# Kernel optimization log

Measured on AMD Instinct MI355X. Metric: run time of the kernel, lower is better.

## Reference

```python
import jax, jax.numpy as jnp
import numpy as np

B, N, HID = 1, 2048, 1024
H, WK, WV = 16, 64, 64
DH = HID // H  # 64


def setup_inputs() -> dict:
    key = jax.random.key(0)
    ks = jax.random.split(key, 10)
    s = 0.02
    return {
        "hidden_states": jax.random.normal(ks[0], (B, N, HID), jnp.float32),
        "attention_mask": jnp.ones((B, N), jnp.float32),
        "Wq": jax.random.normal(ks[1], (HID, HID), jnp.float32) * s,
        "bq": jnp.zeros((HID,), jnp.float32),
        "Wk": jax.random.normal(ks[2], (HID, HID), jnp.float32) * s,
        "bk": jnp.zeros((HID,), jnp.float32),
        "Wv": jax.random.normal(ks[3], (HID, HID), jnp.float32) * s,
        "bv": jnp.zeros((HID,), jnp.float32),
        # Conv1D(2*WK+1, DH, bias=False): weight [nx=DH, nf=2*WK+1]
        "W_rel_k": jax.random.normal(ks[4], (DH, 2 * WK + 1), jnp.float32) * s,
        # relative_pos_val: [2*WV+1, DH]
        "W_rel_v": jax.random.normal(ks[5], (2 * WV + 1, DH), jnp.float32) * s,
    }


def _attention(hidden_states, attention_mask, Wq, bq, Wk, bk, Wv, bv, W_rel_k, W_rel_v):
    b, n, _ = hidden_states.shape

    def heads(x):  # [B,N,HID] -> [B,H,N,DH]
        return x.reshape(b, n, H, DH).transpose(0, 2, 1, 3)

    q = heads(hidden_states @ Wq + bq)
    k = heads(hidden_states @ Wk + bk)
    v = heads(hidden_states @ Wv + bv)

    scores = jnp.einsum("bhid,bhjd->bhij", q, k)  # [B,H,N,N]

    # --- relative-position key bias: bias[i, j] = q_i . w_{j-i+WK} for |j-i|<=WK ---
    a_k = jnp.einsum("bhid,dw->bhiw", q, W_rel_k)  # [B,H,N,2*WK+1]
    rows = jnp.arange(n)
    slot = rows[None, :] - rows[:, None] + WK       # [N,N] relative slot j-i+WK
    valid_k = (slot >= 0) & (slot <= 2 * WK)
    bias = a_k[:, :, rows[:, None], jnp.clip(slot, 0, 2 * WK)]  # [B,H,N,N]
    scores = scores + jnp.where(valid_k, bias, 0.0)

    scores = scores / np.float32(np.sqrt(DH))  # temperature == 1.0

    # extended attention mask: (1 - mask) * dtype_min added to scores
    ext = (1.0 - attention_mask)[:, None, None, :] * jnp.finfo(scores.dtype).min
    scores = scores + ext

    probs = jax.nn.softmax(scores, axis=-1)  # [B,H,N,N]

    ctx = jnp.einsum("bhij,bhjd->bhid", probs, v)  # [B,H,N,DH]

    # --- relative-position value: band[i, r] = probs[i, i-WV+r]; ctx += band @ W_rel_v ---
    offs = jnp.arange(2 * WV + 1)
    kpos = rows[:, None] - WV + offs[None, :]       # [N, 2*WV+1] absolute key position
    valid_v = (kpos >= 0) & (kpos < n)
    band = probs[:, :, rows[:, None], jnp.clip(kpos, 0, n - 1)]  # [B,H,N,2*WV+1]
    band = jnp.where(valid_v, band, 0.0)
    ctx = ctx + jnp.einsum("bhiw,wd->bhid", band, W_rel_v)

    # merge heads -> [B,N,HID]
    return ctx.transpose(0, 2, 1, 3).reshape(b, n, HID)


def reference(hidden_states, attention_mask, Wq, bq, Wk, bk, Wv, bv, W_rel_k, W_rel_v):
    return _attention(hidden_states, attention_mask, Wq, bq, Wk, bk, Wv, bv, W_rel_k, W_rel_v)
```

## Files before the change

### kernel.cpp

```cpp
#include <hip/hip_runtime.h>
#include <hip/hip_bf16.h>

#define NSEQ 2048
#define HIDDIM 1024
#define NH 16
#define DHEAD 64
#define NW 129
#define AKS 132

typedef float          f32x4 __attribute__((ext_vector_type(4)));
typedef _Float16       f16x4 __attribute__((ext_vector_type(4)));
typedef _Float16       f16x8 __attribute__((ext_vector_type(8)));
typedef unsigned short u16x8 __attribute__((ext_vector_type(8)));
typedef unsigned short u16;

__device__ __forceinline__ float b2f(u16 u){ return __uint_as_float(((unsigned)u) << 16); }
__device__ __forceinline__ float ld_any(const void* p, long idx, int flag){
  return flag ? b2f(((const u16*)p)[idx]) : ((const float*)p)[idx];
}
__device__ __forceinline__ int dtype_flag(const void* mask){
  return (((const unsigned*)mask)[0] == 0x3F800000u) ? 0 : 1;
}

#define GLOAD_LDS16(gp, lp) \
  __builtin_amdgcn_global_load_lds((const __attribute__((address_space(1))) unsigned int*)(gp), \
                                   (__attribute__((address_space(3))) unsigned int*)(lp), 16, 0, 0)

static const size_t OFF_Q    = 0;
static const size_t OFF_K    = (size_t)4  << 20;
static const size_t OFF_VT   = (size_t)8  << 20;
static const size_t OFF_WT   = (size_t)12 << 20;
static const size_t OFF_AK   = (size_t)18 << 20;
static const size_t OFF_M    = OFF_AK + (size_t)NH * NSEQ * AKS * 4;
static const size_t OFF_L    = OFF_M + (size_t)2 * NH * NSEQ * 4;
static const size_t OFF_CTXP = OFF_L + (size_t)2 * NH * NSEQ * 4;
static const size_t OFF_HSF  = OFF_CTXP + (size_t)2 * NSEQ * HIDDIM * 4;
static const size_t OFF_BIAS = OFF_HSF + (size_t)NSEQ * HIDDIM * 2;
static const size_t OFF_EXT  = OFF_BIAS + 3 * 1024 * 4;
static const size_t OFF_WRKT = OFF_EXT + (size_t)NSEQ * 4;
static const size_t OFF_WRVT = OFF_WRKT + (size_t)144 * 72 * 2;

__global__ void prep_kernel(const void* __restrict__ hs, const void* __restrict__ mask,
                            const void* __restrict__ bq, const void* __restrict__ bk,
                            const void* __restrict__ bv, const void* __restrict__ wrk,
                            const void* __restrict__ wrv,
                            const void* __restrict__ Wq, const void* __restrict__ Wk,
                            const void* __restrict__ Wv,
                            _Float16* __restrict__ hsf, float* __restrict__ biasf,
                            float* __restrict__ extf, _Float16* __restrict__ wrkT16,
                            _Float16* __restrict__ wrvT16, _Float16* __restrict__ Wt){
  __shared__ __attribute__((aligned(16))) _Float16 tile[64][65];
  const int flag = dtype_flag(mask);
  const int b = blockIdx.x;
  const int t = threadIdx.x;
  if (b < 1024){
    const long base = (long)(b * 256 + t) * 8;
    f16x8 o;
    if (flag){
      u16x8 v = *(const u16x8*)((const u16*)hs + base);
#pragma unroll
      for (int e = 0; e < 8; e++) o[e] = (_Float16)b2f(v[e]);
    } else {
      f32x4 a = *(const f32x4*)((const float*)hs + base);
      f32x4 c = *(const f32x4*)((const float*)hs + base + 4);
#pragma unroll
      for (int e = 0; e < 4; e++){ o[e] = (_Float16)a[e]; o[4 + e] = (_Float16)c[e]; }
    }
    *(f16x8*)(hsf + base) = o;
    return;
  }
  if (b < 1121){
    const int idx = (b - 1024) * 256 + t;
    if (idx < 1024)            biasf[idx] = ld_any(bq, idx, flag);
    else if (idx < 2048)       biasf[idx] = ld_any(bk, idx - 1024, flag);
    else if (idx < 3072)       biasf[idx] = ld_any(bv, idx - 2048, flag);
    else if (idx < 5120)       extf[idx - 3072] = (1.f - ld_any(mask, idx - 3072, flag)) * -1.0e30f;
    else if (idx < 5120 + 144 * 72){
      int i2 = idx - 5120;
      int w = i2 / 72, d = i2 - w * 72;
      wrkT16[i2] = (w < NW && d < 64) ? (_Float16)ld_any(wrk, (long)d * NW + w, flag) : (_Float16)0.f;
    } else if (idx < 5120 + 144 * 72 + 64 * 144){
      int i3 = idx - (5120 + 144 * 72);
      int d = i3 / 144, w = i3 - d * 144;
      wrvT16[i3] = (w < NW) ? (_Float16)ld_any(wrv, (long)w * 64 + d, flag) : (_Float16)0.f;
    }
    return;
  }
  const int b2 = b - 1121;
  const int z = b2 >> 8, rem = b2 & 255;
  const void* src = (z == 0) ? Wq : ((z == 1) ? Wk : Wv);
  _Float16* dst = Wt + (size_t)z * 1024 * 1024;
  const int o0 = (rem & 15) * 64, k0 = (rem >> 4) * 64;
#pragma unroll
  for (int c = 0; c < 2; c++){
    int idx = t + 256 * c;
    int r = idx >> 3, c8 = (idx & 7) * 8;
    long off = (long)(k0 + r) * 1024 + o0 + c8;
    if (flag){
      u16x8 v = *(const u16x8*)((const u16*)src + off);
#pragma unroll
      for (int e = 0; e < 8; e++) tile[r][c8 + e] = (_Float16)b2f(v[e]);
    } else {
      f32x4 a = *(const f32x4*)((const float*)src + off);
      f32x4 bb = *(const f32x4*)((const float*)src + off + 4);
#pragma unroll
      for (int e = 0; e < 4; e++){ tile[r][c8 + e] = (_Float16)a[e]; tile[r][c8 + 4 + e] = (_Float16)bb[e]; }
    }
  }
  __syncthreads();
#pragma unroll
  for (int c = 0; c < 2; c++){
    int idx = t + 256 * c;
    int orow = idx >> 3, k8 = (idx & 7) * 8;
    f16x8 v;
#pragma unroll
    for (int e = 0; e < 8; e++) v[e] = tile[k8 + e][orow];
    *(f16x8*)(dst + (size_t)(o0 + orow) * 1024 + k0 + k8) = v;
  }
}

__launch_bounds__(512, 4)
__global__ void qkv_kernel(const _Float16* __restrict__ hsf, const _Float16* __restrict__ Wt,
                           const float* __restrict__ biasf, const _Float16* __restrict__ wrkT16,
                           _Float16* __restrict__ Qf, _Float16* __restrict__ Kf,
                           _Float16* __restrict__ Vtf, float* __restrict__ akp){
  __shared__ __attribute__((aligned(16))) _Float16 As[2 * 64 * 64];
  __shared__ __attribute__((aligned(16))) _Float16 Bs[2 * 128 * 64];
  const int z = blockIdx.z;
  const _Float16* Wz = Wt + (size_t)z * 1024 * 1024;
  const int o0 = blockIdx.x * 128, m0 = blockIdx.y * 64;
  const int t = threadIdx.x, lane = t & 63, wave = t >> 6;
  const int wm = wave >> 2, wn = wave & 3;
  const int q = lane >> 4, ln = lane & 15;

  auto stage = [&](int nb, int k0){
    {
      const int row = t >> 3, slot = t & 7;
      const int c8 = slot ^ (row & 7);
      GLOAD_LDS16(hsf + (size_t)(m0 + row) * 1024 + k0 + (c8 << 3),
                  (_Float16*)As + nb * 4096 + (wave << 9));
    }
#pragma unroll
    for (int p = 0; p < 2; p++){
      const int g = p * 512 + t;
      const int row = g >> 3, slot = g & 7;
      const int c8 = slot ^ (row & 7);
      GLOAD_LDS16(Wz + (size_t)(o0 + row) * 1024 + k0 + (c8 << 3),
                  (_Float16*)Bs + nb * 8192 + ((p * 8 + wave) << 9));
    }
  };

  f32x4 acc[2][2];
#pragma unroll
  for (int a = 0; a < 2; a++)
#pragma unroll
    for (int b = 0; b < 2; b++) acc[a][b] = (f32x4){0.f, 0.f, 0.f, 0.f};

  stage(0, 0);
  __syncthreads();
  int cur = 0;
  for (int k0 = 0; k0 < 1024; k0 += 64){
    if (k0 + 64 < 1024) stage(cur ^ 1, k0 + 64);
    const _Float16* Ac = (const _Float16*)As + cur * 4096;
    const _Float16* Bc = (const _Float16*)Bs + cur * 8192;
    __builtin_amdgcn_s_setprio(1);
#pragma unroll
    for (int ks = 0; ks < 2; ks++){
      f16x8 af[2], bf[2];
#pragma unroll
      for (int mt = 0; mt < 2; mt++){
        int row = wm * 32 + mt * 16 + ln;
        af[mt] = *(const f16x8*)&Ac[(row << 6) + (((ks * 4 + q) ^ (row & 7)) << 3)];
      }
#pragma unroll
      for (int nt = 0; nt < 2; nt++){
        int row = wn * 32 + nt * 16 + ln;
        bf[nt] = *(const f16x8*)&Bc[(row << 6) + (((ks * 4 + q) ^ (row & 7)) << 3)];
      }
#pragma unroll
      for (int mt = 0; mt < 2; mt++)
#pragma unroll
        for (int nt = 0; nt < 2; nt++)
          acc[mt][nt] = __builtin_amdgcn_mfma_f32_16x16x32_f16(af[mt], bf[nt], acc[mt][nt], 0, 0, 0);
    }
    __builtin_amdgcn_s_setprio(0);
    __syncthreads();
    cur ^= 1;
  }
  const float sc = (z == 0) ? 0.125f : 1.0f;
  _Float16* Qs = (_Float16*)As;
  _Float16* Wl = (_Float16*)Bs;
#pragma unroll
  for (int nt = 0; nt < 2; nt++){
    int ol = wn * 32 + nt * 16 + ln;
    int o = o0 + ol;
    float bval = biasf[z * 1024 + o];
    int hh = o >> 6, dd = o & 63;
#pragma unroll
    for (int mt = 0; mt < 2; mt++){
      int ml = wm * 32 + mt * 16 + q * 4;
      int nb = m0 + ml;
      if (z == 2){
        f16x4 pk;
#pragma unroll
        for (int r = 0; r < 4; r++) pk[r] = (_Float16)(acc[mt][nt][r] + bval);
        *(f16x4*)(Vtf + (size_t)(hh * 64 + dd) * 2048 + nb) = pk;
      } else {
        _Float16* dstp = (z == 0) ? Qf : Kf;
#pragma unroll
        for (int r = 0; r < 4; r++){
          _Float16 v16 = (_Float16)((acc[mt][nt][r] + bval) * sc);
          dstp[(size_t)(hh * 2048 + nb + r) * 64 + dd] = v16;
          if (z == 0) Qs[(ol >> 6) * 4096 + (ml + r) * 64 + dd] = v16;
        }
      }
    }
  }
  if (z == 0){
    {
      const f16x8* srcv = (const f16x8*)wrkT16;
      f16x8* dstv = (f16x8*)Wl;
#pragma unroll
      for (int c = 0; c < 3; c++){
        int v = c * 512 + t;
        if (v < 144 * 72 / 8) dstv[v] = srcv[v];
      }
    }
    __syncthreads();
    const int hl = wave >> 2, mb = wave & 3;
    f16x8 afr[2];
#pragma unroll
    for (int ks = 0; ks < 2; ks++)
      afr[ks] = *(const f16x8*)&Qs[hl * 4096 + (mb * 16 + ln) * 64 + ks * 32 + q * 8];
    f32x4 aacc[9];
#pragma unroll
    for (int b = 0; b < 9; b++) aacc[b] = (f32x4){0.f, 0.f, 0.f, 0.f};
#pragma unroll
    for (int nt = 0; nt < 9; nt++){
      f16x8 bfr0 = *(const f16x8*)&Wl[(nt * 16 + ln) * 72 + q * 8];
      f16x8 bfr1 = *(const f16x8*)&Wl[(nt * 16 + ln) * 72 + 32 + q * 8];
      aacc[nt] = __builtin_amdgcn_mfma_f32_16x16x32_f16(afr[0], bfr0, aacc[nt], 0, 0, 0);
      aacc[nt] = __builtin_amdgcn_mfma_f32_16x16x32_f16(afr[1], bfr1, aacc[nt], 0, 0, 0);
    }
    const int hg = blockIdx.x * 2 + hl;
#pragma unroll
    for (int nt = 0; nt < 9; nt++){
      int w = nt * 16 + ln;
      if (w > 128) continue;
      int ib = m0 + mb * 16 + q * 4;
#pragma unroll
      for (int r = 0; r < 4; r++)
        akp[(size_t)(hg * 2048 + ib + r) * AKS + w] = aacc[nt][r];
    }
  }
}

__launch_bounds__(256, 4)
__global__ void flash_kernel(const float* __restrict__ extf,
                             const _Float16* __restrict__ Qf, const _Float16* __restrict__ Kf,
                             const _Float16* __restrict__ Vtf, float* akm,
                             _Float16* __restrict__ ctxpart, float* __restrict__ mws,
                             float* __restrict__ lws){
  __shared__ __attribute__((aligned(16))) _Float16 Ks[2 * 64 * 64];
  __shared__ __attribute__((aligned(16))) _Float16 Vts[2 * 64 * 64];
  __shared__ __attribute__((aligned(16))) float Exts[1024];
  __shared__ int eflags[4];
  const int h = blockIdx.x, qt = blockIdx.y, jh = blockIdx.z;
  const int t = threadIdx.x, lane = t & 63, wave = t >> 6;
  const int q = lane >> 4, ln = lane & 15;
  const int ibase = qt * 64 + wave * 16;
  const int i = ibase + ln;
  const int jb = jh * 1024;
  const int phase = (h + 3 * qt + 8 * jh) & 15;

  auto stageK = [&](int nb, int jn){
#pragma unroll
    for (int p = 0; p < 2; p++){
      const int g = p * 256 + t;
      const int row = g >> 3, slot = g & 7;
      const int col8 = slot ^ (row & 7);
      GLOAD_LDS16(Kf + (((size_t)(h * 2048 + jn + row)) << 6) + (col8 << 3),
                  (_Float16*)Ks + nb * 4096 + ((p * 4 + wave) << 9));
    }
  };
  auto stageV = [&](int nb, int jn){
#pragma unroll
    for (int p = 0; p < 2; p++){
      const int g = p * 256 + t;
      const int row = g >> 3, slot = g & 7;
      const int col8 = slot ^ (row & 7);
      GLOAD_LDS16(Vtf + (((size_t)(h * 64 + row)) << 11) + jn + (col8 << 3),
                  (_Float16*)Vts + nb * 4096 + ((p * 4 + wave) << 9));
    }
  };

  const int ds7 = ln & 7;
  const _Float16* kb0 = (const _Float16*)Ks + (ln << 6) + ((q ^ ds7) << 3);
  const _Float16* kb1 = (const _Float16*)Ks + (ln << 6) + (((q + 4) ^ ds7) << 3);
  const _Float16* vb0 = (const _Float16*)Vts + (ln << 6) + (((0 | (q >> 1)) ^ ds7) << 3) + ((q & 1) << 2);
  const _Float16* vb1 = (const _Float16*)Vts + (ln << 6) + (((2 | (q >> 1)) ^ ds7) << 3) + ((q & 1) << 2);
  const _Float16* vb2 = (const _Float16*)Vts + (ln << 6) + (((4 | (q >> 1)) ^ ds7) << 3) + ((q & 1) << 2);
  const _Float16* vb3 = (const _Float16*)Vts + (ln << 6) + (((6 | (q >> 1)) ^ ds7) << 3) + ((q & 1) << 2);

  f16x8 qfrag[2];
  {
    const _Float16* qrow = Qf + (size_t)(h * 2048 + i) * 64;
    qfrag[0] = *(const f16x8*)(qrow + q * 8);
    qfrag[1] = *(const f16x8*)(qrow + 32 + q * 8);
  }
  f32x4 accc[4];
#pragma unroll
  for (int dt = 0; dt < 4; dt++) accc[dt] = (f32x4){0.f, 0.f, 0.f, 0.f};
  float m_i = -1.0e30f, l_i = 0.f;
  float* akrow = akm + (size_t)(h * 2048 + i) * AKS;
  f32x4 s[4];

  auto qk = [&](int PK){
    __builtin_amdgcn_s_setprio(1);
#pragma unroll
    for (int mt = 0; mt < 4; mt++){
      f16x8 kf0 = *(const f16x8*)(kb0 + PK * 4096 + mt * 1024);
      f16x8 kf1 = *(const f16x8*)(kb1 + PK * 4096 + mt * 1024);
      f32x4 zz = (f32x4){0.f, 0.f, 0.f, 0.f};
      zz = __builtin_amdgcn_mfma_f32_16x16x32_f16(kf0, qfrag[0], zz, 0, 0, 0);
      zz = __builtin_amdgcn_mfma_f32_16x16x32_f16(kf1, qfrag[1], zz, 0, 0, 0);
      s[mt] = zz;
    }
    __builtin_amdgcn_s_setprio(0);
  };

  auto jof = [&](int x){ return jb + ((x + phase) & 15) * 64; };

  bool nz = false;
#pragma unroll
  for (int c = 0; c < 4; c++){
    float e = extf[jb + c * 256 + t];
    Exts[c * 256 + t] = e;
    nz |= (e != 0.f);
  }
  {
    unsigned long long bz = __ballot(nz);
    if (lane == 0) eflags[wave] = (bz != 0ull) ? 1 : 0;
  }
  stageK(0, jof(0));
  __syncthreads();
  const bool extNZ = (eflags[0] | eflags[1] | eflags[2] | eflags[3]) != 0;
  stageV(0, jof(0));
  stageK(1, jof(1));
  qk(0);
  __syncthreads();

  auto body = [&](int t_, int PV_, int PK1, bool last){
    const int j0 = jof(t_);
    if (!last){
      stageV(PK1, jof(t_ + 1));
      if (t_ < 14) stageK(PV_, jof(t_ + 2));
    }
    const bool band = (j0 <= ibase + 79) && (j0 + 63 >= ibase - 64);
    const int je = (t_ + phase) & 15;
    if (band){
#pragma unroll
      for (int mt = 0; mt < 4; mt++){
        f32x4 ev = *(const f32x4*)&Exts[je * 64 + mt * 16 + (q << 2)];
#pragma unroll
        for (int r = 0; r < 4; r++){
          float x = s[mt][r];
          int w = j0 + mt * 16 + (q << 2) + r - i + 64;
          if ((unsigned)w <= 128u){
            x = x + akrow[w] + ev[r];
            akrow[w] = x;
          } else {
            x = x + ev[r];
          }
          s[mt][r] = x;
        }
      }
    } else if (extNZ){
#pragma unroll
      for (int mt = 0; mt < 4; mt++){
        f32x4 ev = *(const f32x4*)&Exts[je * 64 + mt * 16 + (q << 2)];
#pragma unroll
        for (int r = 0; r < 4; r++) s[mt][r] += ev[r];
      }
    }
    float a0 = fmaxf(fmaxf(s[0][0], s[0][1]), fmaxf(s[0][2], s[0][3]));
    float a1 = fmaxf(fmaxf(s[1][0], s[1][1]), fmaxf(s[1][2], s[1][3]));
    float a2 = fmaxf(fmaxf(s[2][0], s[2][1]), fmaxf(s[2][2], s[2][3]));
    float a3 = fmaxf(fmaxf(s[3][0], s[3][1]), fmaxf(s[3][2], s[3][3]));
    float tmax = fmaxf(fmaxf(a0, a1), fmaxf(a2, a3));
    tmax = fmaxf(tmax, __shfl_xor(tmax, 16, 64));
    tmax = fmaxf(tmax, __shfl_xor(tmax, 32, 64));
    float mnew = fmaxf(m_i, tmax);
    if (!__all(tmax <= m_i)){
      float alpha = __expf(m_i - mnew);
      l_i *= alpha;
#pragma unroll
      for (int dt = 0; dt < 4; dt++)
#pragma unroll
        for (int r = 0; r < 4; r++) accc[dt][r] *= alpha;
    }
    m_i = mnew;
    float ps[4][4];
#pragma unroll
    for (int mt = 0; mt < 4; mt++)
#pragma unroll
      for (int r = 0; r < 4; r++) ps[mt][r] = __expf(s[mt][r] - mnew);
    f16x4 pf[4];
#pragma unroll
    for (int mt = 0; mt < 4; mt++)
#pragma unroll
      for (int r = 0; r < 4; r++) pf[mt][r] = (_Float16)ps[mt][r];
    float t0 = (ps[0][0] + ps[0][1]) + (ps[0][2] + ps[0][3]);
    float t1 = (ps[1][0] + ps[1][1]) + (ps[1][2] + ps[1][3]);
    float t2 = (ps[2][0] + ps[2][1]) + (ps[2][2] + ps[2][3]);
    float t3 = (ps[3][0] + ps[3][1]) + (ps[3][2] + ps[3][3]);
    float tsum = (t0 + t1) + (t2 + t3);
    tsum += __shfl_xor(tsum, 16, 64);
    tsum += __shfl_xor(tsum, 32, 64);
    l_i += tsum;
    if (!last) qk(PK1);
    __builtin_amdgcn_s_setprio(1);
#pragma unroll
    for (int dt = 0; dt < 4; dt++){
      f16x4 vf0 = *(const f16x4*)(vb0 + PV_ * 4096 + dt * 1024);
      f16x4 vf1 = *(const f16x4*)(vb1 + PV_ * 4096 + dt * 1024);
      f16x4 vf2 = *(const f16x4*)(vb2 + PV_ * 4096 + dt * 1024);
      f16x4 vf3 = *(const f16x4*)(vb3 + PV_ * 4096 + dt * 1024);
      accc[dt] = __builtin_amdgcn_mfma_f32_16x16x16f16(vf0, pf[0], accc[dt], 0, 0, 0);
      accc[dt] = __builtin_amdgcn_mfma_f32_16x16x16f16(vf1, pf[1], accc[dt], 0, 0, 0);
      accc[dt] = __builtin_amdgcn_mfma_f32_16x16x16f16(vf2, pf[2], accc[dt], 0, 0, 0);
      accc[dt] = __builtin_amdgcn_mfma_f32_16x16x16f16(vf3, pf[3], accc[dt], 0, 0, 0);
    }
    __builtin_amdgcn_s_setprio(0);
    __syncthreads();
  };

  for (int tt = 0; tt < 8; tt++){
    body(2 * tt,     0, 1, false);
    body(2 * tt + 1, 1, 0, tt == 7);
  }

  _Float16* cdst = ctxpart + (size_t)jh * NSEQ * HIDDIM;
#pragma unroll
  for (int dt = 0; dt < 4; dt++){
    f16x4 pk;
#pragma unroll
    for (int r = 0; r < 4; r++) pk[r] = (_Float16)accc[dt][r];
    *(f16x4*)(cdst + (size_t)i * 1024 + h * 64 + dt * 16 + q * 4) = pk;
  }
  if (q == 0){
    mws[jh * NH * NSEQ + h * 2048 + i] = m_i;
    lws[jh * NH * NSEQ + h * 2048 + i] = l_i;
  }
}

__launch_bounds__(256, 2)
__global__ void finish_kernel(const float* __restrict__ sband, const float* __restrict__ mws,
                              const float* __restrict__ lws, const _Float16* __restrict__ wrvT16,
                              const _Float16* __restrict__ ctxpart, float* __restrict__ out){
  __shared__ __attribute__((aligned(16))) _Float16 WrvT[64 * 144];
  __shared__ __attribute__((aligned(16))) _Float16 pT[144 * 72];
  __shared__ __attribute__((aligned(16))) float sM[64], sIL[64], sC0[64], sC1[64];
  const int qt = blockIdx.x, h = blockIdx.y;
  const int i0 = qt * 64;
  const int t = threadIdx.x, lane = t & 63, wave = t >> 6;
  const int q = lane >> 4, ln = lane & 15;
  {
    const f16x8* srcv = (const f16x8*)wrvT16;
    f16x8* dstv = (f16x8*)WrvT;
#pragma unroll
    for (int c = 0; c < 5; c++){
      int v = c * 256 + t;
      if (v < 64 * 144 / 8) dstv[v] = srcv[v];
    }
  }
  if (t < 64){
    int i = i0 + t;
    float m0 = mws[h * 2048 + i],            m1 = mws[NH * NSEQ + h * 2048 + i];
    float l0 = lws[h * 2048 + i],            l1 = lws[NH * NSEQ + h * 2048 + i];
    float M = fmaxf(m0, m1);
    float a0 = __expf(m0 - M), a1 = __expf(m1 - M);
    float L = a0 * l0 + a1 * l1;
    float iL = 1.f / L;
    sM[t] = M; sIL[t] = iL; sC0[t] = a0 * iL; sC1[t] = a1 * iL;
  }
  __syncthreads();
  for (int ii = 0; ii < 16; ii++){
    int il = wave * 16 + ii;
    float Mv = sM[il], ILv = sIL[il];
    const float* srow = sband + (size_t)(h * 2048 + i0 + il) * AKS;
#pragma unroll
    for (int c = 0; c < 3; c++){
      int w = lane + 64 * c;
      if (w < 144){
        float p = (w < NW) ? __expf(srow[w] - Mv) * ILv : 0.f;
        pT[w * 72 + il] = (_Float16)p;
      }
    }
  }
  __syncthreads();
  f32x4 acc[4];
#pragma unroll
  for (int mt = 0; mt < 4; mt++) acc[mt] = (f32x4){0.f, 0.f, 0.f, 0.f};
#pragma unroll
  for (int ks = 0; ks < 9; ks++){
    f16x4 bfr;
#pragma unroll
    for (int j = 0; j < 4; j++) bfr[j] = pT[(ks * 16 + q * 4 + j) * 72 + wave * 16 + ln];
#pragma unroll
    for (int mt = 0; mt < 4; mt++){
      f16x4 afr = *(const f16x4*)&WrvT[(mt * 16 + ln) * 144 + ks * 16 + q * 4];
      acc[mt] = __builtin_amdgcn_mfma_f32_16x16x16f16(afr, bfr, acc[mt], 0, 0, 0);
    }
  }
  const int i = i0 + wave * 16 + ln;
  const float c0 = sC0[wave * 16 + ln], c1 = sC1[wave * 16 + ln];
  const _Float16* p0 = ctxpart;
  const _Float16* p1 = ctxpart + (size_t)NSEQ * HIDDIM;
#pragma unroll
  for (int mt = 0; mt < 4; mt++){
    size_t off = (size_t)i * 1024 + h * 64 + mt * 16 + q * 4;
    f16x4 A0 = *(const f16x4*)(p0 + off);
    f16x4 A1 = *(const f16x4*)(p1 + off);
    f32x4 o4;
#pragma unroll
    for (int r = 0; r < 4; r++) o4[r] = c0 * (float)A0[r] + c1 * (float)A1[r] + acc[mt][r];
    *(f32x4*)(out + off) = o4;
  }
}

extern "C" void kernel_launch(void* const* d_in, const int* in_sizes, int n_in,
                              void* d_out, int out_size, void* d_ws, size_t ws_size,
                              hipStream_t stream){
  const void* hs   = d_in[0];
  const void* mask = d_in[1];
  const void* Wq   = d_in[2];
  const void* bq   = d_in[3];
  const void* Wk   = d_in[4];
  const void* bk   = d_in[5];
  const void* Wv   = d_in[6];
  const void* bv   = d_in[7];
  const void* Wrk  = d_in[8];
  const void* Wrv  = d_in[9];
  float* out = (float*)d_out;

  char* ws = (char*)d_ws;
  _Float16* Qf    = (_Float16*)(ws + OFF_Q);
  _Float16* Kf    = (_Float16*)(ws + OFF_K);
  _Float16* Vtf   = (_Float16*)(ws + OFF_VT);
  _Float16* Wt    = (_Float16*)(ws + OFF_WT);
  float*    akp   = (float*)   (ws + OFF_AK);
  float*    mp    = (float*)   (ws + OFF_M);
  float*    lp    = (float*)   (ws + OFF_L);
  _Float16* ctxp  = (_Float16*)(ws + OFF_CTXP);
  _Float16* hsf   = (_Float16*)(ws + OFF_HSF);
  float*    biasf = (float*)   (ws + OFF_BIAS);
  float*    extf  = (float*)   (ws + OFF_EXT);
  _Float16* wrkT16= (_Float16*)(ws + OFF_WRKT);
  _Float16* wrvT16= (_Float16*)(ws + OFF_WRVT);

  prep_kernel     <<<dim3(1889),       256, 0, stream>>>(hs, mask, bq, bk, bv, Wrk, Wrv,
                                                         Wq, Wk, Wv,
                                                         hsf, biasf, extf, wrkT16, wrvT16, Wt);
  qkv_kernel      <<<dim3(8, 32, 3),   512, 0, stream>>>(hsf, Wt, biasf, wrkT16,
                                                         Qf, Kf, Vtf, akp);
  flash_kernel    <<<dim3(16, 32, 2),  256, 0, stream>>>(extf, Qf, Kf, Vtf, akp, ctxp, mp, lp);
  finish_kernel   <<<dim3(32, 16),     256, 0, stream>>>(akp, mp, lp, wrvT16, ctxp, out);
}
```

Measured before the change: 173.9 us.

## Fuse split-KV merge and relative-value epilogue into flash kernel via atomic counter

Removes the separate finish kernel. Each flash block bumps an atomic counter per (head, query tile), and the block that arrives second merges the two key halves. It uses its own accumulator straight from registers and reads only the other half's partial context, then applies the relative-position value band GEMM and writes the output. The counters are zeroed in the prep kernel, and the shared memory is rebuilt as one byte buffer so the epilogue can reuse it. This saves a kernel launch and one partial-context read. In exchange, half the flash blocks carry a longer tail, and the code now relies on thread fences and atomics for cross-block ordering.

```diff
diff --git a/kernel.cpp b/kernel.cpp
--- a/kernel.cpp
+++ b/kernel.cpp
@@ -39,6 +39,7 @@
 static const size_t OFF_EXT  = OFF_BIAS + 3 * 1024 * 4;
 static const size_t OFF_WRKT = OFF_EXT + (size_t)NSEQ * 4;
 static const size_t OFF_WRVT = OFF_WRKT + (size_t)144 * 72 * 2;
+static const size_t OFF_CNT  = OFF_WRVT + (size_t)64 * 144 * 2;
 
 __global__ void prep_kernel(const void* __restrict__ hs, const void* __restrict__ mask,
                             const void* __restrict__ bq, const void* __restrict__ bk,
@@ -48,7 +49,8 @@
                             const void* __restrict__ Wv,
                             _Float16* __restrict__ hsf, float* __restrict__ biasf,
                             float* __restrict__ extf, _Float16* __restrict__ wrkT16,
-                            _Float16* __restrict__ wrvT16, _Float16* __restrict__ Wt){
+                            _Float16* __restrict__ wrvT16, _Float16* __restrict__ Wt,
+                            int* __restrict__ cnt){
   __shared__ __attribute__((aligned(16))) _Float16 tile[64][65];
   const int flag = dtype_flag(mask);
   const int b = blockIdx.x;
@@ -69,7 +71,7 @@
     *(f16x8*)(hsf + base) = o;
     return;
   }
-  if (b < 1121){
+  if (b < 1123){
     const int idx = (b - 1024) * 256 + t;
     if (idx < 1024)            biasf[idx] = ld_any(bq, idx, flag);
     else if (idx < 2048)       biasf[idx] = ld_any(bk, idx - 1024, flag);
@@ -83,10 +85,12 @@
       int i3 = idx - (5120 + 144 * 72);
       int d = i3 / 144, w = i3 - d * 144;
       wrvT16[i3] = (w < NW) ? (_Float16)ld_any(wrv, (long)w * 64 + d, flag) : (_Float16)0.f;
+    } else if (idx < 5120 + 144 * 72 + 64 * 144 + 512){
+      cnt[idx - (5120 + 144 * 72 + 64 * 144)] = 0;
     }
     return;
   }
-  const int b2 = b - 1121;
+  const int b2 = b - 1123;
   const int z = b2 >> 8, rem = b2 & 255;
   const void* src = (z == 0) ? Wq : ((z == 1) ? Wk : Wv);
   _Float16* dst = Wt + (size_t)z * 1024 * 1024;
@@ -260,11 +264,13 @@
                              const _Float16* __restrict__ Qf, const _Float16* __restrict__ Kf,
                              const _Float16* __restrict__ Vtf, float* akm,
                              _Float16* __restrict__ ctxpart, float* __restrict__ mws,
-                             float* __restrict__ lws){
-  __shared__ __attribute__((aligned(16))) _Float16 Ks[2 * 64 * 64];
-  __shared__ __attribute__((aligned(16))) _Float16 Vts[2 * 64 * 64];
-  __shared__ __attribute__((aligned(16))) float Exts[1024];
-  __shared__ int eflags[4];
+                             float* __restrict__ lws, const _Float16* __restrict__ wrvT16,
+                             float* __restrict__ out, int* __restrict__ cnt){
+  __shared__ __attribute__((aligned(16))) char smem[39712];
+  _Float16* Ks  = (_Float16*)smem;
+  _Float16* Vts = (_Float16*)(smem + 16384);
+  float*   Exts = (float*)(smem + 32768);
+  int*   eflags = (int*)(smem + 36864);
   const int h = blockIdx.x, qt = blockIdx.y, jh = blockIdx.z;
   const int t = threadIdx.x, lane = t & 63, wave = t >> 6;
   const int q = lane >> 4, ln = lane & 15;
@@ -280,7 +286,7 @@
       const int row = g >> 3, slot = g & 7;
       const int col8 = slot ^ (row & 7);
       GLOAD_LDS16(Kf + (((size_t)(h * 2048 + jn + row)) << 6) + (col8 << 3),
-                  (_Float16*)Ks + nb * 4096 + ((p * 4 + wave) << 9));
+                  Ks + nb * 4096 + ((p * 4 + wave) << 9));
     }
   };
   auto stageV = [&](int nb, int jn){
@@ -290,17 +296,17 @@
       const int row = g >> 3, slot = g & 7;
       const int col8 = slot ^ (row & 7);
       GLOAD_LDS16(Vtf + (((size_t)(h * 64 + row)) << 11) + jn + (col8 << 3),
-                  (_Float16*)Vts + nb * 4096 + ((p * 4 + wave) << 9));
+                  Vts + nb * 4096 + ((p * 4 + wave) << 9));
     }
   };
 
   const int ds7 = ln & 7;
-  const _Float16* kb0 = (const _Float16*)Ks + (ln << 6) + ((q ^ ds7) << 3);
-  const _Float16* kb1 = (const _Float16*)Ks + (ln << 6) + (((q + 4) ^ ds7) << 3);
-  const _Float16* vb0 = (const _Float16*)Vts + (ln << 6) + (((0 | (q >> 1)) ^ ds7) << 3) + ((q & 1) << 2);
-  const _Float16* vb1 = (const _Float16*)Vts + (ln << 6) + (((2 | (q >> 1)) ^ ds7) << 3) + ((q & 1) << 2);
-  const _Float16* vb2 = (const _Float16*)Vts + (ln << 6) + (((4 | (q >> 1)) ^ ds7) << 3) + ((q & 1) << 2);
-  const _Float16* vb3 = (const _Float16*)Vts + (ln << 6) + (((6 | (q >> 1)) ^ ds7) << 3) + ((q & 1) << 2);
+  const _Float16* kb0 = Ks + (ln << 6) + ((q ^ ds7) << 3);
+  const _Float16* kb1 = Ks + (ln << 6) + (((q + 4) ^ ds7) << 3);
+  const _Float16* vb0 = Vts + (ln << 6) + (((0 | (q >> 1)) ^ ds7) << 3) + ((q & 1) << 2);
+  const _Float16* vb1 = Vts + (ln << 6) + (((2 | (q >> 1)) ^ ds7) << 3) + ((q & 1) << 2);
+  const _Float16* vb2 = Vts + (ln << 6) + (((4 | (q >> 1)) ^ ds7) << 3) + ((q & 1) << 2);
+  const _Float16* vb3 = Vts + (ln << 6) + (((6 | (q >> 1)) ^ ds7) << 3) + ((q & 1) << 2);
 
   f16x8 qfrag[2];
   {
@@ -452,19 +458,19 @@
     mws[jh * NH * NSEQ + h * 2048 + i] = m_i;
     lws[jh * NH * NSEQ + h * 2048 + i] = l_i;
   }
-}
-
-__launch_bounds__(256, 2)
-__global__ void finish_kernel(const float* __restrict__ sband, const float* __restrict__ mws,
-                              const float* __restrict__ lws, const _Float16* __restrict__ wrvT16,
-                              const _Float16* __restrict__ ctxpart, float* __restrict__ out){
-  __shared__ __attribute__((aligned(16))) _Float16 WrvT[64 * 144];
-  __shared__ __attribute__((aligned(16))) _Float16 pT[144 * 72];
-  __shared__ __attribute__((aligned(16))) float sM[64], sIL[64], sC0[64], sC1[64];
-  const int qt = blockIdx.x, h = blockIdx.y;
-  const int i0 = qt * 64;
-  const int t = threadIdx.x, lane = t & 63, wave = t >> 6;
-  const int q = lane >> 4, ln = lane & 15;
+
+  __threadfence();
+  __syncthreads();
+  int* flagS = (int*)(smem + 39680);
+  if (t == 0) *flagS = (atomicAdd(&cnt[h * 32 + qt], 1) == 1) ? 1 : 0;
+  __syncthreads();
+  if (!*flagS) return;
+  __threadfence();
+
+  _Float16* WrvT = (_Float16*)smem;
+  _Float16* pT   = (_Float16*)(smem + 18432);
+  float* sM  = (float*)(smem + 39168);
+  float* sIL = (float*)(smem + 39424);
   {
     const f16x8* srcv = (const f16x8*)wrvT16;
     f16x8* dstv = (f16x8*)WrvT;
@@ -474,21 +480,20 @@
       if (v < 64 * 144 / 8) dstv[v] = srcv[v];
     }
   }
-  if (t < 64){
-    int i = i0 + t;
-    float m0 = mws[h * 2048 + i],            m1 = mws[NH * NSEQ + h * 2048 + i];
-    float l0 = lws[h * 2048 + i],            l1 = lws[NH * NSEQ + h * 2048 + i];
-    float M = fmaxf(m0, m1);
-    float a0 = __expf(m0 - M), a1 = __expf(m1 - M);
-    float L = a0 * l0 + a1 * l1;
-    float iL = 1.f / L;
-    sM[t] = M; sIL[t] = iL; sC0[t] = a0 * iL; sC1[t] = a1 * iL;
-  }
-  __syncthreads();
+  const int jo = 1 - jh;
+  float m_o = mws[jo * NH * NSEQ + h * 2048 + i];
+  float l_o = lws[jo * NH * NSEQ + h * 2048 + i];
+  float M = fmaxf(m_i, m_o);
+  float a_own = __expf(m_i - M), a_oth = __expf(m_o - M);
+  float iL = 1.f / (a_own * l_i + a_oth * l_o);
+  float c_own = a_own * iL, c_oth = a_oth * iL;
+  if (q == 0){ sM[wave * 16 + ln] = M; sIL[wave * 16 + ln] = iL; }
+  __syncthreads();
+  const int i0 = qt * 64;
   for (int ii = 0; ii < 16; ii++){
     int il = wave * 16 + ii;
     float Mv = sM[il], ILv = sIL[il];
-    const float* srow = sband + (size_t)(h * 2048 + i0 + il) * AKS;
+    const float* srow = akm + (size_t)(h * 2048 + i0 + il) * AKS;
 #pragma unroll
     for (int c = 0; c < 3; c++){
       int w = lane + 64 * c;
@@ -499,9 +504,9 @@
     }
   }
   __syncthreads();
-  f32x4 acc[4];
-#pragma unroll
-  for (int mt = 0; mt < 4; mt++) acc[mt] = (f32x4){0.f, 0.f, 0.f, 0.f};
+  f32x4 cacc[4];
+#pragma unroll
+  for (int mt = 0; mt < 4; mt++) cacc[mt] = (f32x4){0.f, 0.f, 0.f, 0.f};
 #pragma unroll
   for (int ks = 0; ks < 9; ks++){
     f16x4 bfr;
@@ -510,21 +515,18 @@
 #pragma unroll
     for (int mt = 0; mt < 4; mt++){
       f16x4 afr = *(const f16x4*)&WrvT[(mt * 16 + ln) * 144 + ks * 16 + q * 4];
-      acc[mt] = __builtin_amdgcn_mfma_f32_16x16x16f16(afr, bfr, acc[mt], 0, 0, 0);
-    }
-  }
-  const int i = i0 + wave * 16 + ln;
-  const float c0 = sC0[wave * 16 + ln], c1 = sC1[wave * 16 + ln];
-  const _Float16* p0 = ctxpart;
-  const _Float16* p1 = ctxpart + (size_t)NSEQ * HIDDIM;
+      cacc[mt] = __builtin_amdgcn_mfma_f32_16x16x16f16(afr, bfr, cacc[mt], 0, 0, 0);
+    }
+  }
+  const _Float16* pOth = ctxpart + (size_t)jo * NSEQ * HIDDIM;
 #pragma unroll
   for (int mt = 0; mt < 4; mt++){
     size_t off = (size_t)i * 1024 + h * 64 + mt * 16 + q * 4;
-    f16x4 A0 = *(const f16x4*)(p0 + off);
-    f16x4 A1 = *(const f16x4*)(p1 + off);
+    f16x4 Ao = *(const f16x4*)(pOth + off);
     f32x4 o4;
 #pragma unroll
-    for (int r = 0; r < 4; r++) o4[r] = c0 * (float)A0[r] + c1 * (float)A1[r] + acc[mt][r];
+    for (int r = 0; r < 4; r++)
+      o4[r] = c_own * accc[mt][r] + c_oth * (float)Ao[r] + cacc[mt][r];
     *(f32x4*)(out + off) = o4;
   }
 }
@@ -558,12 +560,14 @@
   float*    extf  = (float*)   (ws + OFF_EXT);
   _Float16* wrkT16= (_Float16*)(ws + OFF_WRKT);
   _Float16* wrvT16= (_Float16*)(ws + OFF_WRVT);
-
-  prep_kernel     <<<dim3(1889),       256, 0, stream>>>(hs, mask, bq, bk, bv, Wrk, Wrv,
+  int*      cntp  = (int*)     (ws + OFF_CNT);
+
+  prep_kernel     <<<dim3(1891),       256, 0, stream>>>(hs, mask, bq, bk, bv, Wrk, Wrv,
                                                          Wq, Wk, Wv,
-                                                         hsf, biasf, extf, wrkT16, wrvT16, Wt);
+                                                         hsf, biasf, extf, wrkT16, wrvT16, Wt,
+                                                         cntp);
   qkv_kernel      <<<dim3(8, 32, 3),   512, 0, stream>>>(hsf, Wt, biasf, wrkT16,
                                                          Qf, Kf, Vtf, akp);
-  flash_kernel    <<<dim3(16, 32, 2),  256, 0, stream>>>(extf, Qf, Kf, Vtf, akp, ctxp, mp, lp);
-  finish_kernel   <<<dim3(32, 16),     256, 0, stream>>>(akp, mp, lp, wrvT16, ctxp, out);
+  flash_kernel    <<<dim3(16, 32, 2),  256, 0, stream>>>(extf, Qf, Kf, Vtf, akp, ctxp, mp, lp,
+                                                         wrvT16, out, cntp);
 }
```

Result: slower. 381.2 us (+119.2%).
